# Performance work log

Hardware: AMD Instinct MI355X
Metric: run time of the kernel (lower is better)

## Reference

```python
import jax, jax.numpy as jnp
import numpy as np

GROUPS = 8
EPS = 1e-5


def group_norm(x, gamma, beta):
    # x: [B,H,W,C]; normalize per group over (H, W, C/g)
    B, H, W, C = x.shape
    g = GROUPS
    xg = x.reshape(B, H, W, g, C // g)
    mean = jnp.mean(xg, axis=(1, 2, 4), keepdims=True)
    var = jnp.var(xg, axis=(1, 2, 4), keepdims=True)
    xg = (xg - mean) / jnp.sqrt(var + EPS)
    return gamma * xg.reshape(B, H, W, C) + beta


def setup_inputs() -> dict:
    key = jax.random.key(0)
    ks = jax.random.split(key, 6)
    B, H, W, C = 8, 64, 64, 128
    s = 1.0 / np.sqrt(C)
    return {
        "x": jax.random.normal(ks[0], (B, H, W, C), jnp.float32),
        "gamma": jnp.ones((C,), jnp.float32),
        "beta": jnp.zeros((C,), jnp.float32),
        "wq": jax.random.normal(ks[1], (C, C), jnp.float32) * s,
        "bq": jnp.zeros((C,), jnp.float32),
        "wk": jax.random.normal(ks[2], (C, C), jnp.float32) * s,
        "bk": jnp.zeros((C,), jnp.float32),
        "wv": jax.random.normal(ks[3], (C, C), jnp.float32) * s,
        "bv": jnp.zeros((C,), jnp.float32),
        "wp": jax.random.normal(ks[4], (C, C), jnp.float32) * s,
        "bp": jnp.zeros((C,), jnp.float32),
    }


def reference(x, gamma, beta, wq, bq, wk, bk, wv, bv, wp, bp):
    B, H, W, C = x.shape
    scale = jnp.asarray(C, jnp.float32) ** -0.5
    xn = group_norm(x, gamma, beta)  # note: residual uses normalized input (as in source)
    N = H * W
    xf = xn.reshape(B, N, C)
    q = xf @ wq + bq
    k = xf @ wk + bk
    v = xf @ wv + bv
    attn = jnp.einsum('bnc,bmc->bnm', q, k) * scale  # [B, N, N]
    attn = jax.nn.softmax(attn, axis=-1)
    out = jnp.einsum('bnm,bmc->bnc', attn, v)
    out = out @ wp + bp
    return (xf + out).reshape(B, H, W, C)
```

## Files before the change

kernel.cpp:

```cpp
#include <hip/hip_runtime.h>
#include <hip/hip_bf16.h>

#define B_ 8
#define N_ 4096
#define C_ 128
#define EPSV 1e-5f
#define SPLIT 2
#define KVB 64

using bf8   = __attribute__((ext_vector_type(8))) short;
using u16x8 = __attribute__((ext_vector_type(8))) ushort;
using f32x4 = __attribute__((ext_vector_type(4))) float;

__device__ __forceinline__ ushort f2b(float f) {
  __hip_bfloat16 h = __float2bfloat16(f);
  return *reinterpret_cast<ushort*>(&h);
}
__device__ __forceinline__ float b2f(ushort u) {
  union { float f; unsigned x; } t; t.x = ((unsigned)u) << 16; return t.f;
}

__device__ __forceinline__ void gll16(const void* g, void* l) {
  __builtin_amdgcn_global_load_lds((const __attribute__((address_space(1))) void*)g,
                                   (__attribute__((address_space(3))) void*)l,
                                   16, 0, 0);
}

__global__ __launch_bounds__(256) void gnw(const float* __restrict__ x,
                                           const float* __restrict__ wq,
                                           const float* __restrict__ wk,
                                           const float* __restrict__ wv,
                                           const float* __restrict__ wp,
                                           float2* __restrict__ part,
                                           ushort* __restrict__ wt) {
  if (blockIdx.y >= 64) {
    const int widx = blockIdx.y - 64;
    const float* w = (widx == 0) ? wq : (widx == 1) ? wk : (widx == 2) ? wv : wp;
    ushort* o = wt + widx * 16384;
    const int r  = blockIdx.x * 16 + (threadIdx.x >> 4);
    const int c0 = (threadIdx.x & 15) << 3;
    const float4 v0 = *reinterpret_cast<const float4*>(w + (size_t)r * C_ + c0);
    const float4 v1 = *reinterpret_cast<const float4*>(w + (size_t)r * C_ + c0 + 4);
    const float vv[8] = {v0.x, v0.y, v0.z, v0.w, v1.x, v1.y, v1.z, v1.w};
    #pragma unroll
    for (int j = 0; j < 8; ++j) {
      const int n = c0 + j;
      const int el = (r & 7) | ((((r >> 3)) ^ (n & 7)) << 3);
      o[(size_t)n * C_ + el] = f2b(vv[j]);
    }
    return;
  }
  const int bg = blockIdx.y;
  const int b = bg >> 3, g = bg & 7;
  const int chunk = blockIdx.x;
  const float* xp = x + (size_t)b * N_ * C_ + g * 16;
  float s = 0.f, s2 = 0.f;
  const int base4 = chunk * 2048;
  for (int i = threadIdx.x; i < 2048; i += 256) {
    const int idx = base4 + i;
    const int n = idx >> 2, c4 = (idx & 3) << 2;
    const float4 v = *reinterpret_cast<const float4*>(xp + (size_t)n * C_ + c4);
    s  += v.x + v.y + v.z + v.w;
    s2 += v.x*v.x + v.y*v.y + v.z*v.z + v.w*v.w;
  }
  #pragma unroll
  for (int off = 32; off; off >>= 1) { s += __shfl_down(s, off); s2 += __shfl_down(s2, off); }
  __shared__ float red[8];
  const int wid = threadIdx.x >> 6;
  if ((threadIdx.x & 63) == 0) { red[wid] = s; red[4 + wid] = s2; }
  __syncthreads();
  if (threadIdx.x == 0)
    part[bg * 8 + chunk] = make_float2(red[0]+red[1]+red[2]+red[3],
                                       red[4]+red[5]+red[6]+red[7]);
}

__device__ __forceinline__ void block_mrs(const float2* part, int b, int tid,
                                          float2* sp, float* mrs) {
  if (tid < 64) sp[tid] = part[b * 64 + tid];
  __syncthreads();
  if (tid < 8) {
    float s = 0.f, s2 = 0.f;
    #pragma unroll
    for (int c = 0; c < 8; ++c) { s += sp[tid*8+c].x; s2 += sp[tid*8+c].y; }
    const float inv = 1.f / 65536.f;
    const float m = s * inv;
    const float var = s2 * inv - m * m;
    mrs[tid*2]   = m;
    mrs[tid*2+1] = rsqrtf(var + EPSV);
  }
  __syncthreads();
}

__global__ __launch_bounds__(256) void qkv_fused(const float* __restrict__ x,
                                                 const float2* __restrict__ part,
                                                 const float* __restrict__ gamma,
                                                 const float* __restrict__ beta,
                                                 const ushort* __restrict__ wt,
                                                 const float* __restrict__ bq,
                                                 const float* __restrict__ bk,
                                                 const float* __restrict__ bv,
                                                 ushort* __restrict__ qb, ushort* __restrict__ kb,
                                                 ushort* __restrict__ vtb) {
  __shared__ ushort A[64][128];
  __shared__ ushort Bt[128][128];
  __shared__ float2 sp[64];
  __shared__ float mrs[16];
  const int m0 = blockIdx.x * 64;
  const int tid = threadIdx.x;
  const int wid = tid >> 6, lane = tid & 63;
  block_mrs(part, m0 >> 12, tid, sp, mrs);
  for (int i = tid; i < 1024; i += 256) {
    const int row = i >> 4, c = (i & 15) << 3;
    const int grow = m0 + row;
    const float mm = mrs[(c >> 4) * 2], rr = mrs[(c >> 4) * 2 + 1];
    const float4 v0 = *reinterpret_cast<const float4*>(&x[(size_t)grow * C_ + c]);
    const float4 v1 = *reinterpret_cast<const float4*>(&x[(size_t)grow * C_ + c + 4]);
    const float vv[8] = {v0.x, v0.y, v0.z, v0.w, v1.x, v1.y, v1.z, v1.w};
    u16x8 u;
    #pragma unroll
    for (int j = 0; j < 8; ++j)
      u[j] = f2b((vv[j] - mm) * rr * gamma[c+j] + beta[c+j]);
    const int el = ((c >> 3) ^ (row & 7)) << 3;
    *reinterpret_cast<u16x8*>(&A[row][el]) = u;
  }
  const int wm = wid >> 1, wn = wid & 1;
  const int lr = lane & 15, lk = lane >> 4;
  const float qscale = 0.12751749f;

  #pragma unroll 1
  for (int j = 0; j < 3; ++j) {
    const ushort* wtj = wt + j * 16384;
    const float* bias = (j == 0) ? bq : (j == 1) ? bk : bv;
    __syncthreads();
    {
      ushort* bt0 = &Bt[0][0];
      #pragma unroll
      for (int c8 = 0; c8 < 8; ++c8) {
        const int ch = wid * 8 + c8;
        gll16(wtj + ch * 512 + lane * 8, bt0 + ch * 512);
      }
    }
    __syncthreads();
    f32x4 acc[2][4] = {};
    #pragma unroll
    for (int ks = 0; ks < 4; ++ks) {
      const int g0 = ks * 4 + lk;
      bf8 af[2], bfv[4];
      #pragma unroll
      for (int mi = 0; mi < 2; ++mi) {
        const int row = wm * 32 + mi * 16 + lr;
        af[mi] = *reinterpret_cast<const bf8*>(&A[row][(g0 ^ (row & 7)) << 3]);
      }
      #pragma unroll
      for (int ni = 0; ni < 4; ++ni) {
        const int n = wn * 64 + ni * 16 + lr;
        bfv[ni] = *reinterpret_cast<const bf8*>(&Bt[n][(g0 ^ (n & 7)) << 3]);
      }
      #pragma unroll
      for (int mi = 0; mi < 2; ++mi)
        #pragma unroll
        for (int ni = 0; ni < 4; ++ni)
          acc[mi][ni] = __builtin_amdgcn_mfma_f32_16x16x32_bf16(af[mi], bfv[ni], acc[mi][ni], 0, 0, 0);
    }
    if (j < 2) {
      ushort* out = (j == 0) ? qb : kb;
      const float sc = (j == 0) ? qscale : 1.0f;
      #pragma unroll
      for (int mi = 0; mi < 2; ++mi)
        #pragma unroll
        for (int ni = 0; ni < 4; ++ni)
          #pragma unroll
          for (int r = 0; r < 4; ++r) {
            const int row = m0 + wm * 32 + mi * 16 + lk * 4 + r;
            const int col = wn * 64 + ni * 16 + lr;
            out[(size_t)row * C_ + col] = f2b((acc[mi][ni][r] + bias[col]) * sc);
          }
    } else {
      #pragma unroll
      for (int mi = 0; mi < 2; ++mi)
        #pragma unroll
        for (int ni = 0; ni < 4; ++ni) {
          const int rowb = m0 + wm * 32 + mi * 16 + lk * 4;
          const int col  = wn * 64 + ni * 16 + lr;
          const int bb = rowb >> 12, nn = rowb & 4095;
          const int o  = nn & 63;
          const int op = (o & 0x23) | ((o & 0x0C) << 1) | ((o & 0x10) >> 2);
          const int nnp = (nn & ~63) | op;
          const float bv2 = bias[col];
          ushort4 u;
          u.x = f2b(acc[mi][ni][0] + bv2);
          u.y = f2b(acc[mi][ni][1] + bv2);
          u.z = f2b(acc[mi][ni][2] + bv2);
          u.w = f2b(acc[mi][ni][3] + bv2);
          *reinterpret_cast<ushort4*>(&vtb[((size_t)bb * C_ + col) * N_ + nnp]) = u;
        }
    }
  }
}

__global__ __launch_bounds__(256, 2) void attn_fwd(const ushort* __restrict__ q,
                                                   const ushort* __restrict__ k,
                                                   const ushort* __restrict__ vt,
                                                   ushort* __restrict__ Op,
                                                   float* __restrict__ lsum) {
  extern __shared__ ushort smem[];
  const int bid = blockIdx.x;
  const int b   = bid & 7;
  const int qi  = (bid >> 3) & 31;
  const int z   = bid >> 8;
  const int q0  = qi * 128;
  const int tid = threadIdx.x;
  const int w = tid >> 6, lane = tid & 63;
  const int lr = lane & 15, lk = lane >> 4;
  const ushort* qb = q  + (size_t)b * N_ * C_;
  const ushort* kb = k  + (size_t)b * N_ * C_;
  const ushort* vb = vt + (size_t)b * C_ * N_;

  bf8 qf[2][4];
  #pragma unroll
  for (int h = 0; h < 2; ++h) {
    const int qrow = q0 + w * 32 + h * 16 + lr;
    #pragma unroll
    for (int ks = 0; ks < 4; ++ks)
      qf[h][ks] = *reinterpret_cast<const bf8*>(&qb[(size_t)qrow * C_ + ks * 32 + lk * 8]);
  }

  bf8 onesf;
  #pragma unroll
  for (int j = 0; j < 8; ++j) onesf[j] = (short)0x3F80;

  f32x4 oacc[2][8] = {};
  f32x4 accl[2] = {};

  const int krow_in = lane >> 4;
  const int kslot   = lane & 15;
  const int vrow_in = lane >> 3;
  const int vslot   = lane & 7;

  const int t0 = z * (64 / SPLIT);
  const int t1 = (z + 1) * (64 / SPLIT);

  auto STAGE = [&](int sel, int kt) {
    const int kv0 = kt * KVB;
    ushort* Kd = smem + sel * 8192;
    ushort* Vd = smem + 16384 + sel * 8192;
    #pragma unroll
    for (int j = 0; j < 4; ++j) {
      const int m = w * 4 + j;
      const int krow = m * 4 + krow_in;
      gll16(kb + (size_t)(kv0 + krow) * C_ + ((kslot ^ (krow & 7)) << 3),
            Kd + m * 512);
      const int vrow = m * 8 + vrow_in;
      gll16(vb + (size_t)vrow * N_ + kv0 + ((vslot ^ (vrow & 7)) << 3),
            Vd + m * 512);
    }
  };

  STAGE(0, t0);
  __builtin_amdgcn_s_setprio(1);
  for (int kt = t0; kt < t1; ++kt) {
    const int cur = (kt - t0) & 1;
    __syncthreads();
    if (kt + 1 < t1) STAGE(cur ^ 1, kt + 1);

    const ushort* Kc = smem + cur * 8192;
    const ushort* Vc = smem + 16384 + cur * 8192;

    f32x4 s[2][4] = {};
    bf8 kf[2][4];
    #pragma unroll
    for (int ni = 0; ni < 4; ++ni) {
      const int n = ni * 16 + lr;
      kf[0][ni] = *reinterpret_cast<const bf8*>(&Kc[n * 128 + ((lk ^ (n & 7)) << 3)]);
    }
    #pragma unroll
    for (int ks = 0; ks < 4; ++ks) {
      const int cb = ks & 1;
      if (ks < 3) {
        const int g1 = (ks + 1) * 4 + lk;
        #pragma unroll
        for (int ni = 0; ni < 4; ++ni) {
          const int n = ni * 16 + lr;
          kf[cb ^ 1][ni] = *reinterpret_cast<const bf8*>(&Kc[n * 128 + ((g1 ^ (n & 7)) << 3)]);
        }
      }
      #pragma unroll
      for (int h = 0; h < 2; ++h)
        #pragma unroll
        for (int ni = 0; ni < 4; ++ni)
          s[h][ni] = __builtin_amdgcn_mfma_f32_16x16x32_bf16(kf[cb][ni], qf[h][ks], s[h][ni], 0, 0, 0);
    }

    bf8 vf[8];
    #pragma unroll
    for (int ni = 0; ni < 8; ++ni) {
      const int d = ni * 16 + lr;
      vf[ni] = *reinterpret_cast<const bf8*>(&Vc[d * 64 + ((lk ^ (d & 7)) << 3)]);
    }

    #pragma unroll
    for (int kss = 0; kss < 2; ++kss) {
      #pragma unroll
      for (int h = 0; h < 2; ++h) {
        bf8 pah;
        #pragma unroll
        for (int hi = 0; hi < 2; ++hi) {
          const f32x4 sv = s[h][kss * 2 + hi];
          #pragma unroll
          for (int r = 0; r < 4; ++r)
            pah[hi * 4 + r] = (short)f2b(__builtin_amdgcn_exp2f(sv[r]));
        }
        accl[h] = __builtin_amdgcn_mfma_f32_16x16x32_bf16(pah, onesf, accl[h], 0, 0, 0);
        #pragma unroll
        for (int ni = 0; ni < 8; ++ni)
          oacc[h][ni] = __builtin_amdgcn_mfma_f32_16x16x32_bf16(pah, vf[ni], oacc[h][ni], 0, 0, 0);
      }
      if (kss == 0) {
        #pragma unroll
        for (int ni = 0; ni < 8; ++ni) {
          const int d = ni * 16 + lr;
          vf[ni] = *reinterpret_cast<const bf8*>(&Vc[d * 64 + (((4 + lk) ^ (d & 7)) << 3)]);
        }
      }
    }
  }
  __builtin_amdgcn_s_setprio(0);

  const size_t zb = (size_t)(z * B_ + b);
  if (lr == 0) {
    #pragma unroll
    for (int h = 0; h < 2; ++h)
      #pragma unroll
      for (int r = 0; r < 4; ++r)
        lsum[zb * N_ + q0 + w * 32 + h * 16 + lk * 4 + r] = accl[h][r];
  }
  ushort* ob = Op + zb * N_ * C_;
  #pragma unroll
  for (int h = 0; h < 2; ++h)
    #pragma unroll
    for (int ni = 0; ni < 8; ++ni)
      #pragma unroll
      for (int r = 0; r < 4; ++r) {
        const int row = q0 + w * 32 + h * 16 + lk * 4 + r;
        ob[(size_t)row * C_ + ni * 16 + lr] = f2b(oacc[h][ni][r]);
      }
}

__global__ __launch_bounds__(256) void proj_res(const ushort* __restrict__ Op,
                                                const float* __restrict__ lsum,
                                                const ushort* __restrict__ wtp,
                                                const float* __restrict__ bias,
                                                const float* __restrict__ x,
                                                const float2* __restrict__ part,
                                                const float* __restrict__ gamma,
                                                const float* __restrict__ beta,
                                                float* __restrict__ outp) {
  __shared__ ushort A[64][128];
  __shared__ ushort Bt[128][128];
  __shared__ float2 sp[64];
  __shared__ float mrs[16];
  const int m0 = blockIdx.x * 64;
  const int tid = threadIdx.x;
  const int wid = tid >> 6, lane = tid & 63;
  const size_t BN = (size_t)B_ * N_;
  block_mrs(part, m0 >> 12, tid, sp, mrs);
  {
    ushort* bt0 = &Bt[0][0];
    #pragma unroll
    for (int c8 = 0; c8 < 8; ++c8) {
      const int ch = wid * 8 + c8;
      gll16(wtp + ch * 512 + lane * 8, bt0 + ch * 512);
    }
  }
  for (int i = tid; i < 1024; i += 256) {
    const int row = i >> 4, c = (i & 15) << 3;
    const size_t grow = m0 + row;
    float l = 0.f;
    #pragma unroll
    for (int zz = 0; zz < SPLIT; ++zz) l += lsum[zz * BN + grow];
    const float inv = 1.f / l;
    float acc8[8] = {};
    #pragma unroll
    for (int zz = 0; zz < SPLIT; ++zz) {
      const u16x8 a = *reinterpret_cast<const u16x8*>(&Op[(zz * BN + grow) * C_ + c]);
      #pragma unroll
      for (int j = 0; j < 8; ++j) acc8[j] += b2f(a[j]);
    }
    u16x8 u;
    #pragma unroll
    for (int j = 0; j < 8; ++j) u[j] = f2b(acc8[j] * inv);
    const int el = ((c >> 3) ^ (row & 7)) << 3;
    *reinterpret_cast<u16x8*>(&A[row][el]) = u;
  }
  __syncthreads();
  const int wm = wid >> 1, wn = wid & 1;
  const int lr = lane & 15, lk = lane >> 4;
  f32x4 acc[2][4] = {};
  #pragma unroll
  for (int ks = 0; ks < 4; ++ks) {
    const int g0 = ks * 4 + lk;
    bf8 af[2], bfv[4];
    #pragma unroll
    for (int mi = 0; mi < 2; ++mi) {
      const int row = wm * 32 + mi * 16 + lr;
      af[mi] = *reinterpret_cast<const bf8*>(&A[row][(g0 ^ (row & 7)) << 3]);
    }
    #pragma unroll
    for (int ni = 0; ni < 4; ++ni) {
      const int n = wn * 64 + ni * 16 + lr;
      bfv[ni] = *reinterpret_cast<const bf8*>(&Bt[n][(g0 ^ (n & 7)) << 3]);
    }
    #pragma unroll
    for (int mi = 0; mi < 2; ++mi)
      #pragma unroll
      for (int ni = 0; ni < 4; ++ni)
        acc[mi][ni] = __builtin_amdgcn_mfma_f32_16x16x32_bf16(af[mi], bfv[ni], acc[mi][ni], 0, 0, 0);
  }
  #pragma unroll
  for (int mi = 0; mi < 2; ++mi)
    #pragma unroll
    for (int ni = 0; ni < 4; ++ni) {
      const int col = wn * 64 + ni * 16 + lr;
      const float gmm = gamma[col], bta = beta[col], bia = bias[col];
      const float mm = mrs[(col >> 4) * 2], rr = mrs[(col >> 4) * 2 + 1];
      #pragma unroll
      for (int r = 0; r < 4; ++r) {
        const int row = m0 + wm * 32 + mi * 16 + lk * 4 + r;
        const float xn = (x[(size_t)row * C_ + col] - mm) * rr * gmm + bta;
        outp[(size_t)row * C_ + col] = xn + acc[mi][ni][r] + bia;
      }
    }
}

extern "C" void kernel_launch(void* const* d_in, const int* in_sizes, int n_in,
                              void* d_out, int out_size, void* d_ws, size_t ws_size,
                              hipStream_t stream) {
  const float* x     = (const float*)d_in[0];
  const float* gamma = (const float*)d_in[1];
  const float* beta  = (const float*)d_in[2];
  const float* wq    = (const float*)d_in[3];
  const float* bq    = (const float*)d_in[4];
  const float* wk    = (const float*)d_in[5];
  const float* bk    = (const float*)d_in[6];
  const float* wv    = (const float*)d_in[7];
  const float* bv    = (const float*)d_in[8];
  const float* wp    = (const float*)d_in[9];
  const float* bp    = (const float*)d_in[10];
  float* outp = (float*)d_out;

  char* ws = (char*)d_ws;
  const size_t MB8 = (size_t)B_ * N_ * C_ * 2;
  float2* part = (float2*)(ws + 512);
  ushort* qb   = (ushort*)(ws + 8192);
  ushort* kb   = (ushort*)(ws + 8192 + MB8);
  ushort* vtb  = (ushort*)(ws + 8192 + 2*MB8);
  ushort* Op   = (ushort*)(ws + 8192 + 3*MB8);
  float*  lsum = (float*)(ws + 8192 + (3 + SPLIT)*MB8);
  ushort* wt   = (ushort*)(ws + 8192 + (3 + SPLIT)*MB8 + (size_t)SPLIT*B_*N_*4);

  gnw<<<dim3(8, 68), 256, 0, stream>>>(x, wq, wk, wv, wp, part, wt);
  qkv_fused<<<512, 256, 0, stream>>>(x, part, gamma, beta, wt,
                                     bq, bk, bv, qb, kb, vtb);
  (void)hipFuncSetAttribute((const void*)attn_fwd,
                            hipFuncAttributeMaxDynamicSharedMemorySize, 65536);
  attn_fwd<<<dim3(32 * B_ * SPLIT), 256, 65536, stream>>>(qb, kb, vtb, Op, lsum);
  proj_res<<<512, 256, 0, stream>>>(Op, lsum, wt + 3 * 16384, bp, x, part, gamma, beta, outp);
}
```

Before: 98.05 us.

## Raise attention split to three and single-buffer V to fit three blocks per CU

The key/value range is now split three ways instead of two, which gives a larger attention grid. V is no longer double-buffered: it is loaded into one shared slot each iteration while K stays double-buffered, and a barrier is added before the V reads. Shared memory drops from 64 KB to 48 KB and launch bounds ask for three blocks per CU, to raise occupancy and parallelism. The cost is an extra barrier per tile, V load latency that is no longer hidden by prefetch, a tighter register budget under the new launch bounds, and one more partial result for the downstream combine to merge.

```diff
diff --git a/kernel.cpp b/kernel.cpp
--- a/kernel.cpp
+++ b/kernel.cpp
@@ -5,7 +5,7 @@
 #define N_ 4096
 #define C_ 128
 #define EPSV 1e-5f
-#define SPLIT 2
+#define SPLIT 3
 #define KVB 64
 
 using bf8   = __attribute__((ext_vector_type(8))) short;
@@ -198,7 +198,7 @@
   }
 }
 
-__global__ __launch_bounds__(256, 2) void attn_fwd(const ushort* __restrict__ q,
+__global__ __launch_bounds__(256, 3) void attn_fwd(const ushort* __restrict__ q,
                                                    const ushort* __restrict__ k,
                                                    const ushort* __restrict__ vt,
                                                    ushort* __restrict__ Op,
@@ -237,34 +237,42 @@
   const int vrow_in = lane >> 3;
   const int vslot   = lane & 7;
 
-  const int t0 = z * (64 / SPLIT);
-  const int t1 = (z + 1) * (64 / SPLIT);
-
-  auto STAGE = [&](int sel, int kt) {
+  const int t0 = (z * 64) / SPLIT;
+  const int t1 = ((z + 1) * 64) / SPLIT;
+
+  auto STAGE_K = [&](int sel, int kt) {
     const int kv0 = kt * KVB;
     ushort* Kd = smem + sel * 8192;
-    ushort* Vd = smem + 16384 + sel * 8192;
     #pragma unroll
     for (int j = 0; j < 4; ++j) {
       const int m = w * 4 + j;
       const int krow = m * 4 + krow_in;
       gll16(kb + (size_t)(kv0 + krow) * C_ + ((kslot ^ (krow & 7)) << 3),
             Kd + m * 512);
+    }
+  };
+  auto STAGE_V = [&](int kt) {
+    const int kv0 = kt * KVB;
+    ushort* Vd = smem + 16384;
+    #pragma unroll
+    for (int j = 0; j < 4; ++j) {
+      const int m = w * 4 + j;
       const int vrow = m * 8 + vrow_in;
       gll16(vb + (size_t)vrow * N_ + kv0 + ((vslot ^ (vrow & 7)) << 3),
             Vd + m * 512);
     }
   };
 
-  STAGE(0, t0);
+  STAGE_K(0, t0);
   __builtin_amdgcn_s_setprio(1);
   for (int kt = t0; kt < t1; ++kt) {
     const int cur = (kt - t0) & 1;
     __syncthreads();
-    if (kt + 1 < t1) STAGE(cur ^ 1, kt + 1);
+    STAGE_V(kt);
+    if (kt + 1 < t1) STAGE_K(cur ^ 1, kt + 1);
 
     const ushort* Kc = smem + cur * 8192;
-    const ushort* Vc = smem + 16384 + cur * 8192;
+    const ushort* Vc = smem + 16384;
 
     f32x4 s[2][4] = {};
     bf8 kf[2][4];
@@ -291,30 +299,42 @@
           s[h][ni] = __builtin_amdgcn_mfma_f32_16x16x32_bf16(kf[cb][ni], qf[h][ks], s[h][ni], 0, 0, 0);
     }
 
-    bf8 vf[8];
-    #pragma unroll
-    for (int ni = 0; ni < 8; ++ni) {
-      const int d = ni * 16 + lr;
-      vf[ni] = *reinterpret_cast<const bf8*>(&Vc[d * 64 + ((lk ^ (d & 7)) << 3)]);
-    }
-
-    #pragma unroll
-    for (int kss = 0; kss < 2; ++kss) {
+    bf8 pa[2][2];
+    #pragma unroll
+    for (int kss = 0; kss < 2; ++kss)
       #pragma unroll
       for (int h = 0; h < 2; ++h) {
-        bf8 pah;
+        bf8 t;
         #pragma unroll
         for (int hi = 0; hi < 2; ++hi) {
           const f32x4 sv = s[h][kss * 2 + hi];
           #pragma unroll
           for (int r = 0; r < 4; ++r)
-            pah[hi * 4 + r] = (short)f2b(__builtin_amdgcn_exp2f(sv[r]));
+            t[hi * 4 + r] = (short)f2b(__builtin_amdgcn_exp2f(sv[r]));
         }
-        accl[h] = __builtin_amdgcn_mfma_f32_16x16x32_bf16(pah, onesf, accl[h], 0, 0, 0);
+        pa[kss][h] = t;
+      }
+    #pragma unroll
+    for (int kss = 0; kss < 2; ++kss)
+      #pragma unroll
+      for (int h = 0; h < 2; ++h)
+        accl[h] = __builtin_amdgcn_mfma_f32_16x16x32_bf16(pa[kss][h], onesf, accl[h], 0, 0, 0);
+
+    __syncthreads();
+
+    bf8 vf[8];
+    #pragma unroll
+    for (int ni = 0; ni < 8; ++ni) {
+      const int d = ni * 16 + lr;
+      vf[ni] = *reinterpret_cast<const bf8*>(&Vc[d * 64 + ((lk ^ (d & 7)) << 3)]);
+    }
+    #pragma unroll
+    for (int kss = 0; kss < 2; ++kss) {
+      #pragma unroll
+      for (int h = 0; h < 2; ++h)
         #pragma unroll
         for (int ni = 0; ni < 8; ++ni)
-          oacc[h][ni] = __builtin_amdgcn_mfma_f32_16x16x32_bf16(pah, vf[ni], oacc[h][ni], 0, 0, 0);
-      }
+          oacc[h][ni] = __builtin_amdgcn_mfma_f32_16x16x32_bf16(pa[kss][h], vf[ni], oacc[h][ni], 0, 0, 0);
       if (kss == 0) {
         #pragma unroll
         for (int ni = 0; ni < 8; ++ni) {
@@ -462,7 +482,7 @@
   qkv_fused<<<512, 256, 0, stream>>>(x, part, gamma, beta, wt,
                                      bq, bk, bv, qb, kb, vtb);
   (void)hipFuncSetAttribute((const void*)attn_fwd,
-                            hipFuncAttributeMaxDynamicSharedMemorySize, 65536);
-  attn_fwd<<<dim3(32 * B_ * SPLIT), 256, 65536, stream>>>(qb, kb, vtb, Op, lsum);
+                            hipFuncAttributeMaxDynamicSharedMemorySize, 49152);
+  attn_fwd<<<dim3(32 * B_ * SPLIT), 256, 49152, stream>>>(qb, kb, vtb, Op, lsum);
   proj_res<<<512, 256, 0, stream>>>(Op, lsum, wt + 3 * 16384, bp, x, part, gamma, beta, outp);
 }
```

Result: slower. 112.2 us (+14.4%).
